# Kernel optimization log

Measured on AMD Instinct MI355X. Metric: run time of the kernel, lower is better.

Reference implementation:

```python
import jax, jax.numpy as jnp
import numpy as np

# static sinkhorn parameters (match SamplesLoss init kwargs)
P = 2
BLUR = 0.05
SCALING = 0.5
DIAMETER = 2.0  # points on the unit sphere => diameter <= 2

# geomloss epsilon_schedule: [diameter^p] + exp(arange(p*log(d), p*log(blur), p*log(scaling))) + [blur^p]
EPS_LIST = (
    [DIAMETER ** P]
    + [float(np.exp(e)) for e in np.arange(P * np.log(DIAMETER), P * np.log(BLUR), P * np.log(SCALING))]
    + [BLUR ** P]
)


def cost(m, n):
    # spherical (geodesic) distance / 2 between unit vectors: acos(<m,n>)/2
    t = jnp.clip(jnp.einsum('bnd,bmd->bnm', m, n), -1.0 + 1e-6, 1.0 - 1e-6)
    return jnp.arccos(t) * 0.5  # (B,N,M)


def softmin(eps, C, wlog):
    # -eps * logsumexp(wlog[B,1,M] - C/eps, axis=2) -> (B,N)
    return -eps * jax.nn.logsumexp(wlog[:, None, :] - C / eps, axis=2)


def log_weights(a):
    return jnp.where(a > 0, jnp.log(jnp.maximum(a, 1e-30)), -1e5)


def setup_inputs() -> dict:
    key = jax.random.key(0)
    kx, ky = jax.random.split(key)
    B, N, M, D = 8, 2048, 2048, 3
    x = jax.random.normal(kx, (B, N, D), dtype=jnp.float32)
    y = jax.random.normal(ky, (B, M, D), dtype=jnp.float32)
    # project onto the unit sphere (spherical cost assumes unit vectors)
    x = x / jnp.linalg.norm(x, axis=-1, keepdims=True)
    y = y / jnp.linalg.norm(y, axis=-1, keepdims=True)
    alpha = jnp.ones((B, N), dtype=jnp.float32) / N
    beta = jnp.ones((B, M), dtype=jnp.float32) / M
    return {"alpha": alpha, "x": x, "beta": beta, "y": y}


def reference(alpha, x, beta, y):
    sg = jax.lax.stop_gradient
    # second argument of each cost is detached, as in the torch code
    C_xx = cost(x, sg(x))
    C_yy = cost(y, sg(y))
    C_xy = cost(x, sg(y))
    C_yx = cost(y, sg(x))
    al = log_weights(alpha)
    bl = log_weights(beta)

    # ---- sinkhorn loop (torch.no_grad section) ----
    Cxx_, Cyy_, Cxy_, Cyx_, al_, bl_ = map(sg, (C_xx, C_yy, C_xy, C_yx, al, bl))
    eps = EPS_LIST[0]
    a_x = softmin(eps, Cxx_, al_)   # OT(a,a) potential on x
    b_y = softmin(eps, Cyy_, bl_)   # OT(b,b) potential on y
    a_y = softmin(eps, Cyx_, al_)   # OT(a,b) potential on y
    b_x = softmin(eps, Cxy_, bl_)   # OT(a,b) potential on x
    for eps in EPS_LIST:  # annealed, symmetrized sinkhorn updates
        at_x = softmin(eps, Cxx_, al_ + a_x / eps)
        bt_y = softmin(eps, Cyy_, bl_ + b_y / eps)
        at_y = softmin(eps, Cyx_, al_ + b_x / eps)
        bt_x = softmin(eps, Cxy_, bl_ + a_y / eps)
        a_x, b_y = 0.5 * (a_x + at_x), 0.5 * (b_y + bt_y)
        a_y, b_x = 0.5 * (a_y + at_y), 0.5 * (b_x + bt_x)

    # ---- last extrapolation, differentiable (eps = blur^p) ----
    eps = EPS_LIST[-1]
    a_x = softmin(eps, C_xx, sg(al + a_x / eps))
    b_y = softmin(eps, C_yy, sg(bl + b_y / eps))
    a_y = softmin(eps, C_yx, sg(al + b_x / eps))
    b_x = softmin(eps, C_xy, sg(bl + a_y / eps))

    # balanced (reach=None), debiased sinkhorn cost -> (B,)
    return jnp.sum(alpha * (b_x - a_x), axis=-1) + jnp.sum(beta * (a_y - b_y), axis=-1)
```

## Files before the change

### kernel.cpp

```cpp
#include <hip/hip_runtime.h>
#include <math.h>

#define BB 8
#define NN 2048
#define L2E 1.4426950408889634f
#define LN2 0.6931471805599453f
#define PI_F 3.14159265358979f
#define CLIP 0.999999f
#define THSC 20860.0f
#define THSCI (1.0f / 20860.0f)

constexpr int TB   = 128;
constexpr int T16  = NN / TB;
constexpr int NXX  = T16 * (T16 + 1) / 2;
constexpr int NT   = 2 * NXX + T16 * T16;
constexpr int SARR = BB * NN;

__device__ __forceinline__ void decode_tile(int bx, int& kind, int& I, int& J) {
    if (bx < NXX) kind = 0;
    else if (bx < 2 * NXX) { kind = 1; bx -= NXX; }
    else { kind = 2; bx -= 2 * NXX; }
    if (kind < 2) {
        int idx = bx; I = 0;
        for (;;) { int len = T16 - I; if (idx < len) { J = I + idx; break; } idx -= len; I++; }
    } else { I = bx >> 4; J = bx & 15; }
}

__device__ __forceinline__ float acos_raw(float d) {
    const float u = fabsf(d);
    float pl = fmaf(u, -0.0187293f, 0.0742610f);
    pl = fmaf(u, pl, -0.2121144f); pl = fmaf(u, pl, 1.5707288f);
    const float rt = __builtin_amdgcn_sqrtf(1.f - u) * pl;
    return (d >= 0.f) ? rt : (PI_F - rt);
}

__device__ __forceinline__ size_t th_off(int g, int wv, int lane) {
    return (size_t)(((g * 4 + wv) * 64 + lane) * 8);
}

__global__ __launch_bounds__(256)
void pack_kernel(const float* __restrict__ alpha, const float* __restrict__ beta,
                 float* __restrict__ gxw, float* __restrict__ gyw,
                 float* __restrict__ Wall, float* __restrict__ Gall,
                 float* __restrict__ out)
{
    const int tid = threadIdx.x;
    const int gid = blockIdx.x * 256 + tid;
    if (blockIdx.x == 0 && tid < BB) out[tid] = 0.f;
    const int o = gid >> 14, i = gid & (SARR - 1);
    const float* w = (o == 0 || o == 3) ? alpha : beta;
    const float v = w[i];
    const float g = ((v > 0.f) ? logf(fmaxf(v, 1e-30f)) : -1e5f) * L2E;
    if (o == 0) gxw[i] = g;
    if (o == 1) gyw[i] = g;
    float m = g;
    m = fmaxf(m, __shfl_xor(m, 1));  m = fmaxf(m, __shfl_xor(m, 2));
    m = fmaxf(m, __shfl_xor(m, 4));  m = fmaxf(m, __shfl_xor(m, 8));
    m = fmaxf(m, __shfl_xor(m, 16)); m = fmaxf(m, __shfl_xor(m, 32));
    __shared__ float wmax[4];
    const int wv = tid >> 6;
    if ((tid & 63) == 0) wmax[wv] = m;
    __syncthreads();
    const int grp = tid >> 7;
    const float G = fmaxf(wmax[grp * 2], wmax[grp * 2 + 1]);
    Wall[gid] = __builtin_amdgcn_exp2f(g - G);
    if ((tid & 127) == 0) Gall[gid >> 7] = G;
}

__global__ __launch_bounds__(256)
void maxes_kernel(const float* __restrict__ x, const float* __restrict__ y,
                  float* __restrict__ Rxx, float* __restrict__ Ryy,
                  float* __restrict__ Rxy, float* __restrict__ Cxy,
                  unsigned short* __restrict__ Theta,
                  const float* __restrict__ Wall, const float* __restrict__ Gall,
                  float2* pAX, float2* pBY, float2* pAY, float2* pBX,
                  float negK, int writeTheta)
{
    __shared__ float4 p1s[TB], p2s[TB];
    __shared__ float colred[4][TB];
    __shared__ float colpart[4][TB];
    int kind, I, J; decode_tile(blockIdx.x, kind, I, J);
    const int b = blockIdx.y, t = threadIdx.x;
    const float* P1 = (kind == 1) ? y : x;
    const float* P2 = (kind == 0) ? x : y;
    const int o1 = (kind == 0) ? 0 : (kind == 1) ? 1 : 3;
    const int o2 = (kind == 0) ? 0 : (kind == 1) ? 1 : 2;
    float2* rowOut = (kind == 0) ? pAX : (kind == 1) ? pBY : pBX;
    float2* colOut = (kind == 0) ? pAX : (kind == 1) ? pBY : pAY;
    const bool diag = (kind < 2) && (I == J);
    const float* W1 = Wall + (size_t)o1 * SARR;
    const float* W2 = Wall + (size_t)o2 * SARR;

    if (t < TB) {
        size_t gi = (size_t)b * NN + (size_t)I * TB + t;
        p1s[t] = make_float4(P1[gi * 3], P1[gi * 3 + 1], P1[gi * 3 + 2], W1[gi]);
    } else {
        int u = t - TB; size_t gi = (size_t)b * NN + (size_t)J * TB + u;
        p2s[u] = make_float4(P2[gi * 3], P2[gi * 3 + 1], P2[gi * 3 + 2], W2[gi]);
    }
    const float G1 = Gall[o1 * 128 + b * T16 + I];
    const float G2 = Gall[o2 * 128 + b * T16 + J];
    __syncthreads();
    const int lane = t & 63, wv = t >> 6, colg = lane & 7, rowg = lane >> 3;
    const int r0 = wv * 32 + rowg * 4;
    unsigned short* Tb = Theta + ((size_t)(b * NT + blockIdx.x) << 14);

    float4 pr[4];
#pragma unroll
    for (int rr = 0; rr < 4; rr++) pr[rr] = p1s[r0 + rr];
    float rmx[4] = {-2.f, -2.f, -2.f, -2.f};
    float cmx[16];
#pragma unroll
    for (int j = 0; j < 16; j++) cmx[j] = -2.f;
    float racc[4] = {0.f, 0.f, 0.f, 0.f};
    float cacc[16];
#pragma unroll
    for (int j = 0; j < 16; j++) cacc[j] = 0.f;

#pragma unroll
    for (int g = 0; g < 8; g++) {
        uint4 outv;
#pragma unroll
        for (int e = 0; e < 2; e++) {
            const int j = g * 2 + e;
            const float4 q = p2s[colg + 8 * j];
            unsigned int lo = 0, hi = 0;
#pragma unroll
            for (int rr = 0; rr < 4; rr++) {
                const float d = fmaf(pr[rr].x, q.x, fmaf(pr[rr].y, q.y, pr[rr].z * q.z));
                rmx[rr] = fmaxf(rmx[rr], d);
                cmx[j] = fmaxf(cmx[j], d);
                if (writeTheta) {
                    const float dc = fminf(fmaxf(d, -CLIP), CLIP);
                    const float th = acos_raw(dc);
                    const unsigned int qv = __float2uint_rn(th * THSC);
                    if (rr == 0) lo = qv;
                    else if (rr == 1) lo |= qv << 16;
                    else if (rr == 2) hi = qv;
                    else hi |= qv << 16;
                    const float em = __builtin_amdgcn_exp2f(th * negK);
                    racc[rr] = fmaf(q.w, em, racc[rr]);
                    cacc[j]  = fmaf(pr[rr].w, em, cacc[j]);
                }
            }
            if (e == 0) { outv.x = lo; outv.y = hi; }
            else        { outv.z = lo; outv.w = hi; }
        }
        if (writeTheta)
            *(uint4*)(Tb + th_off(g, wv, lane)) = outv;
    }

#pragma unroll
    for (int rr = 0; rr < 4; rr++) {
        float v = rmx[rr];
        v = fmaxf(v, __shfl_xor(v, 1)); v = fmaxf(v, __shfl_xor(v, 2));
        v = fmaxf(v, __shfl_xor(v, 4));
        rmx[rr] = v;
    }
    if (colg == 0) {
        float* R = (kind == 0) ? Rxx : (kind == 1) ? Ryy : Rxy;
        const size_t base = ((size_t)b * T16 + J) * NN + (size_t)I * TB + r0;
#pragma unroll
        for (int rr = 0; rr < 4; rr++)
            R[base + rr] = acos_raw(fminf(fmaxf(rmx[rr], -CLIP), CLIP));
    }
#pragma unroll
    for (int j = 0; j < 16; j++) {
        float v = cmx[j];
        v = fmaxf(v, __shfl_xor(v, 8)); v = fmaxf(v, __shfl_xor(v, 16));
        v = fmaxf(v, __shfl_xor(v, 32));
        cmx[j] = v;
    }
    if (rowg == 0) {
#pragma unroll
        for (int j = 0; j < 16; j++) colred[wv][colg + 8 * j] = cmx[j];
    }

    if (writeTheta) {
#pragma unroll
        for (int j = 0; j < 16; j++) {
            float v = cacc[j];
            v += __shfl_xor(v, 8); v += __shfl_xor(v, 16); v += __shfl_xor(v, 32);
            cacc[j] = v;
        }
        if (rowg == 0) {
#pragma unroll
            for (int j = 0; j < 16; j++) colpart[wv][colg + 8 * j] = cacc[j];
        }
#pragma unroll
        for (int rr = 0; rr < 4; rr++) {
            float v = racc[rr];
            v += __shfl_xor(v, 1); v += __shfl_xor(v, 2); v += __shfl_xor(v, 4);
            racc[rr] = v;
        }
        if (colg == 0) {
            const size_t gr = (size_t)J * SARR + (size_t)b * NN + (size_t)I * TB + r0;
#pragma unroll
            for (int rr = 0; rr < 4; rr++)
                rowOut[gr + rr] = make_float2(G2, racc[rr]);
        }
    }

    __syncthreads();
    if (t < TB) {
        const float v = fmaxf(fmaxf(colred[0][t], colred[1][t]),
                              fmaxf(colred[2][t], colred[3][t]));
        const float th = acos_raw(fminf(fmaxf(v, -CLIP), CLIP));
        if (kind == 2) {
            Cxy[((size_t)b * T16 + I) * NN + (size_t)J * TB + t] = th;
        } else if (I != J) {
            float* R = (kind == 0) ? Rxx : Ryy;
            R[((size_t)b * T16 + I) * NN + (size_t)J * TB + t] = th;
        }
        if (writeTheta && !diag) {
            const float pv = colpart[0][t] + colpart[1][t] + colpart[2][t] + colpart[3][t];
            const size_t gc = (size_t)I * SARR + (size_t)b * NN + (size_t)J * TB + t;
            colOut[gc] = make_float2(G1, pv);
        }
    }
}

struct TileArgsT {
    const unsigned short* Theta;
    const float* Wall; const float* Gall;
    const float* Rxx; const float* Ryy; const float* Rxy; const float* Cxy;
    float2* pAX; float2* pBY; float2* pAY; float2* pBX;
};

__global__ __launch_bounds__(256)
void tile_theta_kernel(TileArgsT A, float ieh, float Kq)
{
    __shared__ float2 s1[TB], s2[TB];
    __shared__ float colpart[4][TB];
    int kind, I, J; decode_tile(blockIdx.x, kind, I, J);
    const int b = blockIdx.y, t = threadIdx.x;
    const int lane = t & 63, wv = t >> 6, colg = lane & 7, rowg = lane >> 3;
    const int r0 = wv * 32 + rowg * 4;

    const unsigned short* Tb = A.Theta + ((size_t)(b * NT + blockIdx.x) << 14);
    uint4 tq[8];
#pragma unroll
    for (int g = 0; g < 8; g++) tq[g] = *(const uint4*)(Tb + th_off(g, wv, lane));

    const int o1 = (kind == 0) ? 0 : (kind == 1) ? 1 : 3;
    const int o2 = (kind == 0) ? 0 : (kind == 1) ? 1 : 2;
    float2* rowOut = (kind == 0) ? A.pAX : (kind == 1) ? A.pBY : A.pBX;
    float2* colOut = (kind == 0) ? A.pAX : (kind == 1) ? A.pBY : A.pAY;
    const bool diag = (kind < 2) && (I == J);
    const float* W1 = A.Wall + (size_t)o1 * SARR;
    const float* W2 = A.Wall + (size_t)o2 * SARR;
    const float* Rrow = (kind == 0) ? A.Rxx : (kind == 1) ? A.Ryy : A.Rxy;
    const float* Csrc = (kind == 0) ? A.Rxx : (kind == 1) ? A.Ryy : A.Cxy;

    if (t < TB) {
        size_t gi = (size_t)b * NN + (size_t)I * TB + t;
        s1[t] = make_float2(Rrow[((size_t)b * T16 + J) * NN + (size_t)I * TB + t] * ieh, W1[gi]);
    } else {
        int u = t - TB; size_t gi = (size_t)b * NN + (size_t)J * TB + u;
        s2[u] = make_float2(Csrc[((size_t)b * T16 + I) * NN + (size_t)J * TB + u] * ieh, W2[gi]);
    }
    const float G1 = A.Gall[o1 * 128 + b * T16 + I];
    const float G2 = A.Gall[o2 * 128 + b * T16 + J];
    __syncthreads();

    float srr[4], w1r[4];
#pragma unroll
    for (int rr = 0; rr < 4; rr++) { const float2 v = s1[r0 + rr]; srr[rr] = v.x; w1r[rr] = v.y; }
    float racc[4] = {0.f, 0.f, 0.f, 0.f};
    float cacc[16];
#pragma unroll
    for (int j = 0; j < 16; j++) cacc[j] = 0.f;

    if (diag) {
#pragma unroll
        for (int g = 0; g < 8; g++) {
#pragma unroll
            for (int e = 0; e < 2; e++) {
                const int j = g * 2 + e;
                const unsigned int lo = e ? tq[g].z : tq[g].x;
                const unsigned int hi = e ? tq[g].w : tq[g].y;
                const float2 sv = s2[colg + 8 * j];
                const float thv[4] = {
                    (float)(lo & 0xffffu), (float)(lo >> 16),
                    (float)(hi & 0xffffu), (float)(hi >> 16)
                };
#pragma unroll
                for (int rr = 0; rr < 4; rr++) {
                    const float er = __builtin_amdgcn_exp2f(fmaf(thv[rr], -Kq, srr[rr]));
                    racc[rr] = fmaf(sv.y, er, racc[rr]);
                }
            }
        }
    } else {
#pragma unroll
        for (int g = 0; g < 8; g++) {
#pragma unroll
            for (int e = 0; e < 2; e++) {
                const int j = g * 2 + e;
                const unsigned int lo = e ? tq[g].z : tq[g].x;
                const unsigned int hi = e ? tq[g].w : tq[g].y;
                const float2 sv = s2[colg + 8 * j];
                const float thv[4] = {
                    (float)(lo & 0xffffu), (float)(lo >> 16),
                    (float)(hi & 0xffffu), (float)(hi >> 16)
                };
#pragma unroll
                for (int rr = 0; rr < 4; rr++) {
                    const float er = __builtin_amdgcn_exp2f(fmaf(thv[rr], -Kq, srr[rr]));
                    const float ec = __builtin_amdgcn_exp2f(fmaf(thv[rr], -Kq, sv.x));
                    racc[rr] = fmaf(sv.y, er, racc[rr]);
                    cacc[j]  = fmaf(w1r[rr], ec, cacc[j]);
                }
            }
        }
    }

#pragma unroll
    for (int rr = 0; rr < 4; rr++) {
        float v = racc[rr];
        v += __shfl_xor(v, 1); v += __shfl_xor(v, 2); v += __shfl_xor(v, 4);
        racc[rr] = v;
    }
    if (colg == 0) {
        const size_t gr = (size_t)J * SARR + (size_t)b * NN + (size_t)I * TB + r0;
#pragma unroll
        for (int rr = 0; rr < 4; rr++)
            rowOut[gr + rr] = make_float2(G2 - srr[rr], racc[rr]);
    }
    if (!diag) {
#pragma unroll
        for (int j = 0; j < 16; j++) {
            float v = cacc[j];
            v += __shfl_xor(v, 8); v += __shfl_xor(v, 16); v += __shfl_xor(v, 32);
            cacc[j] = v;
        }
        if (rowg == 0) {
#pragma unroll
            for (int j = 0; j < 16; j++) colpart[wv][colg + 8 * j] = cacc[j];
        }
        __syncthreads();
        if (t < TB) {
            const float v = colpart[0][t] + colpart[1][t] + colpart[2][t] + colpart[3][t];
            const size_t gc = (size_t)I * SARR + (size_t)b * NN + (size_t)J * TB + t;
            colOut[gc] = make_float2(G1 - s2[t].x, v);
        }
    }
}

struct TileArgs {
    const float* x; const float* y;
    const float* Wall; const float* Gall;
    const float* Rxx; const float* Ryy; const float* Rxy; const float* Cxy;
    float2* pAX; float2* pBY; float2* pAY; float2* pBX;
};

__global__ __launch_bounds__(256)
void tile_kernel(TileArgs A, float ieh, float pi_ieh)
{
    __shared__ float4 p1s[TB], p2s[TB];
    __shared__ float srs[TB], scs[TB];
    __shared__ float colpart[4][TB];
    int kind, I, J; decode_tile(blockIdx.x, kind, I, J);
    const int b = blockIdx.y, t = threadIdx.x;
    const float* P1 = (kind == 1) ? A.y : A.x;
    const float* P2 = (kind == 0) ? A.x : A.y;
    const int o1 = (kind == 0) ? 0 : (kind == 1) ? 1 : 3;
    const int o2 = (kind == 0) ? 0 : (kind == 1) ? 1 : 2;
    float2* rowOut = (kind == 0) ? A.pAX : (kind == 1) ? A.pBY : A.pBX;
    float2* colOut = (kind == 0) ? A.pAX : (kind == 1) ? A.pBY : A.pAY;
    const bool diag = (kind < 2) && (I == J);
    const float* W1 = A.Wall + (size_t)o1 * SARR;
    const float* W2 = A.Wall + (size_t)o2 * SARR;
    const float* Rrow = (kind == 0) ? A.Rxx : (kind == 1) ? A.Ryy : A.Rxy;
    const float* Csrc = (kind == 0) ? A.Rxx : (kind == 1) ? A.Ryy : A.Cxy;

    const float K0 = 1.5707288f * ieh, K1 = -0.2121144f * ieh;
    const float K2 = 0.0742610f * ieh, K3 = -0.0187293f * ieh;

    if (t < TB) {
        size_t gi = (size_t)b * NN + (size_t)I * TB + t;
        p1s[t] = make_float4(P1[gi * 3], P1[gi * 3 + 1], P1[gi * 3 + 2], W1[gi]);
        srs[t] = Rrow[((size_t)b * T16 + J) * NN + (size_t)I * TB + t] * ieh;
    } else {
        int u = t - TB; size_t gi = (size_t)b * NN + (size_t)J * TB + u;
        p2s[u] = make_float4(P2[gi * 3], P2[gi * 3 + 1], P2[gi * 3 + 2], W2[gi]);
        scs[u] = Csrc[((size_t)b * T16 + I) * NN + (size_t)J * TB + u] * ieh;
    }
    const float G1 = A.Gall[o1 * 128 + b * T16 + I];
    const float G2 = A.Gall[o2 * 128 + b * T16 + J];
    __syncthreads();

    const int lane = t & 63, wv = t >> 6, colg = lane & 7, rowg = lane >> 3;
    const int r0 = wv * 32 + rowg * 4;
    float4 pr[4]; float srr[4];
#pragma unroll
    for (int rr = 0; rr < 4; rr++) { pr[rr] = p1s[r0 + rr]; srr[rr] = srs[r0 + rr]; }
    float racc[4] = {0.f, 0.f, 0.f, 0.f};
    float cacc[16];
#pragma unroll
    for (int j = 0; j < 16; j++) cacc[j] = 0.f;

#pragma unroll
    for (int j = 0; j < 16; j++) {
        const float4 q = p2s[colg + 8 * j];
        const float sc = scs[colg + 8 * j];
#pragma unroll
        for (int rr = 0; rr < 4; rr++) {
            const float4 p = pr[rr];
            float d = fmaf(p.x, q.x, fmaf(p.y, q.y, p.z * q.z));
            d = fminf(fmaxf(d, -CLIP), CLIP);
            const float u = fabsf(d);
            float pl = fmaf(u, K3, K2); pl = fmaf(u, pl, K1); pl = fmaf(u, pl, K0);
            const float rt = __builtin_amdgcn_sqrtf(1.f - u) * pl;
            const float ach = (d >= 0.f) ? rt : (pi_ieh - rt);
            racc[rr] = fmaf(q.w, __builtin_amdgcn_exp2f(srr[rr] - ach), racc[rr]);
            cacc[j]  = fmaf(p.w, __builtin_amdgcn_exp2f(sc - ach), cacc[j]);
        }
    }

#pragma unroll
    for (int j = 0; j < 16; j++) {
        float v = cacc[j];
        v += __shfl_xor(v, 8); v += __shfl_xor(v, 16); v += __shfl_xor(v, 32);
        cacc[j] = v;
    }
    if (rowg == 0) {
#pragma unroll
        for (int j = 0; j < 16; j++) colpart[wv][colg + 8 * j] = cacc[j];
    }
#pragma unroll
    for (int rr = 0; rr < 4; rr++) {
        float v = racc[rr];
        v += __shfl_xor(v, 1); v += __shfl_xor(v, 2); v += __shfl_xor(v, 4);
        racc[rr] = v;
    }
    if (colg == 0) {
        const size_t gr = (size_t)J * SARR + (size_t)b * NN + (size_t)I * TB + r0;
#pragma unroll
        for (int rr = 0; rr < 4; rr++)
            rowOut[gr + rr] = make_float2(G2 - srr[rr], racc[rr]);
    }
    __syncthreads();
    if (!diag && t < TB) {
        const float v = colpart[0][t] + colpart[1][t] + colpart[2][t] + colpart[3][t];
        const size_t gc = (size_t)I * SARR + (size_t)b * NN + (size_t)J * TB + t;
        colOut[gc] = make_float2(G1 - scs[t], v);
    }
}

__global__ __launch_bounds__(256)
void combine_kernel(const float2* __restrict__ pAX, const float2* __restrict__ pBY,
                    const float2* __restrict__ pAY, const float2* __restrict__ pBX,
                    float* __restrict__ ax, float* __restrict__ by,
                    float* __restrict__ ay, float* __restrict__ bx,
                    const float* __restrict__ gxw, const float* __restrict__ gyw,
                    float* __restrict__ Wall, float* __restrict__ Gall,
                    const float* __restrict__ alpha, const float* __restrict__ beta,
                    float* __restrict__ out,
                    float eps_ln2, float nieL2E, int do_avg, int do_out)
{
    const int tid = threadIdx.x;
    const int gid2 = blockIdx.x * 256 + tid;
    const int row = gid2 >> 1, half = gid2 & 1;
    const int o = row >> 14, i = row & (SARR - 1);
    const float2* P = (o == 0) ? pAX : (o == 1) ? pBY : (o == 2) ? pAY : pBX;
    float* pot = (o == 0) ? ax : (o == 1) ? by : (o == 2) ? ay : bx;
    float2 pr[8];
#pragma unroll
    for (int u = 0; u < 8; u++) pr[u] = P[(size_t)(half * 8 + u) * SARR + i];
    float M = -3.0e38f;
#pragma unroll
    for (int u = 0; u < 8; u++) M = fmaxf(M, (pr[u].y > 0.f) ? pr[u].x : -3.0e38f);
    float S = 0.f;
#pragma unroll
    for (int u = 0; u < 8; u++)
        S += pr[u].y * __builtin_amdgcn_exp2f(fminf(pr[u].x - M, 0.f));
    const float Mo = __shfl_xor(M, 1);
    const float So = __shfl_xor(S, 1);
    const float nm = fmaxf(M, Mo);
    S = S * __builtin_amdgcn_exp2f(M - nm) + So * __builtin_amdgcn_exp2f(Mo - nm);
    S = fmaxf(S, 1e-38f);
    float r = -eps_ln2 * (nm + __builtin_amdgcn_logf(S));
    if (do_avg) r = 0.5f * (r + pot[i]);
    if (half == 0) pot[i] = r;

    const int wv = tid >> 6;
    if (do_out) {
        float c = 0.f;
        if (half == 0) {
            const float w = ((o == 0 || o == 3) ? alpha : beta)[i];
            const float sgn = (o == 0 || o == 1) ? -1.f : 1.f;
            c = sgn * w * r;
        }
        c += __shfl_xor(c, 1);  c += __shfl_xor(c, 2);  c += __shfl_xor(c, 4);
        c += __shfl_xor(c, 8);  c += __shfl_xor(c, 16); c += __shfl_xor(c, 32);
        __shared__ float bs[4];
        if ((tid & 63) == 0) bs[wv] = c;
        __syncthreads();
        if (tid == 0) atomicAdd(&out[i >> 11], bs[0] + bs[1] + bs[2] + bs[3]);
        return;
    }

    const float g = ((o == 0 || o == 3) ? gxw[i] : gyw[i]) + r * nieL2E;
    float m = g;
    m = fmaxf(m, __shfl_xor(m, 1));  m = fmaxf(m, __shfl_xor(m, 2));
    m = fmaxf(m, __shfl_xor(m, 4));  m = fmaxf(m, __shfl_xor(m, 8));
    m = fmaxf(m, __shfl_xor(m, 16)); m = fmaxf(m, __shfl_xor(m, 32));
    __shared__ float wmax[4];
    if ((tid & 63) == 0) wmax[wv] = m;
    __syncthreads();
    const float G = fmaxf(fmaxf(wmax[0], wmax[1]), fmaxf(wmax[2], wmax[3]));
    if (half == 0) Wall[row] = __builtin_amdgcn_exp2f(g - G);
    if (tid == 0) Gall[blockIdx.x] = G;
}

extern "C" void kernel_launch(void* const* d_in, const int* in_sizes, int n_in,
                              void* d_out, int out_size, void* d_ws, size_t ws_size,
                              hipStream_t stream)
{
    const float* alpha = (const float*)d_in[0];
    const float* x     = (const float*)d_in[1];
    const float* beta  = (const float*)d_in[2];
    const float* y     = (const float*)d_in[3];
    float* out = (float*)d_out;
    float* ws  = (float*)d_ws;

    const size_t S = SARR;
    float* gxw  = ws;
    float* gyw  = ws + S;
    float* ax   = ws + 2 * S;
    float* by   = ws + 3 * S;
    float* ay   = ws + 4 * S;
    float* bx   = ws + 5 * S;
    float* Wall = ws + 6 * S;
    float* Gall = ws + 10 * S;
    float* Rxx  = ws + 10 * S + 512;
    float* Ryy  = Rxx + 16 * S;
    float* Rxy  = Ryy + 16 * S;
    float* Cxy  = Rxy + 16 * S;
    float* pb   = Cxy + 16 * S;
    const size_t PSZ = (size_t)SARR * T16;
    float2* pAX = (float2*)pb;
    float2* pBY = pAX + PSZ;
    float2* pAY = pBY + PSZ;
    float2* pBX = pAY + PSZ;

    float* thetaF = pb + (size_t)8 * PSZ;
    unsigned short* Theta = (unsigned short*)thetaF;
    const size_t used_bytes  = (size_t)((char*)thetaF - (char*)ws);
    const size_t theta_bytes = (size_t)BB * NT * 16384 * sizeof(unsigned short);
    const int useTheta = (ws_size >= used_bytes + theta_bytes) ? 1 : 0;

    const float EPS[8] = {4.0f, 4.0f, 1.0f, 0.25f, 0.0625f, 0.015625f, 0.00390625f, 0.0025f};

    pack_kernel<<<(4 * SARR) / 256, 256, 0, stream>>>(alpha, beta, gxw, gyw, Wall, Gall, out);
    const float negK = -0.5f * (1.f / EPS[0]) * L2E;
    maxes_kernel<<<dim3(NT, BB), 256, 0, stream>>>(x, y, Rxx, Ryy, Rxy, Cxy, Theta,
                                                   Wall, Gall, pAX, pBY, pAY, pBX,
                                                   negK, useTheta);

    TileArgsT TT;
    TT.Theta = Theta; TT.Wall = Wall; TT.Gall = Gall;
    TT.Rxx = Rxx; TT.Ryy = Ryy; TT.Rxy = Rxy; TT.Cxy = Cxy;
    TT.pAX = pAX; TT.pBY = pBY; TT.pAY = pAY; TT.pBX = pBX;

    TileArgs TA;
    TA.x = x; TA.y = y; TA.Wall = Wall; TA.Gall = Gall;
    TA.Rxx = Rxx; TA.Ryy = Ryy; TA.Rxy = Rxy; TA.Cxy = Cxy;
    TA.pAX = pAX; TA.pBY = pBY; TA.pAY = pAY; TA.pBX = pBX;

    auto step = [&](float e, float next_e, int avg, int run_tile, int do_out) {
        const float ieh = 0.5f * (1.f / e) * L2E;
        if (run_tile) {
            if (useTheta)
                tile_theta_kernel<<<dim3(NT, BB), 256, 0, stream>>>(TT, ieh, ieh * THSCI);
            else
                tile_kernel<<<dim3(NT, BB), 256, 0, stream>>>(TA, ieh, PI_F * ieh);
        }
        combine_kernel<<<(8 * SARR) / 256, 256, 0, stream>>>(
            pAX, pBY, pAY, pBX, ax, by, ay, bx, gxw, gyw, Wall, Gall,
            alpha, beta, out,
            e * LN2, (1.f / next_e) * L2E, avg, do_out);
    };

    step(EPS[0], EPS[0], 0, useTheta ? 0 : 1, 0);
    for (int k = 0; k < 8; k++) step(EPS[k], (k < 7) ? EPS[k + 1] : EPS[7], 1, 1, 0);
    step(EPS[7], EPS[7], 0, 1, 1);
}
```

Baseline: 415.0 us.

## Process two theta tiles per block, prefetching second tile's loads upfront

Each block of the theta tile kernel now handles two consecutive tiles. It issues the global loads for both tiles' theta data and staging values before computing the first one, so memory latency for the second tile overlaps the first tile's compute. The grid is halved and launch bounds request 3 blocks per CU. Holding both tiles' data in registers raises register pressure, and NT must be even for the pairing to cover every tile.

```diff
diff --git a/kernel.cpp b/kernel.cpp
--- a/kernel.cpp
+++ b/kernel.cpp
@@ -227,41 +227,39 @@
     float2* pAX; float2* pBY; float2* pAY; float2* pBX;
 };
 
-__global__ __launch_bounds__(256)
-void tile_theta_kernel(TileArgsT A, float ieh, float Kq)
-{
-    __shared__ float2 s1[TB], s2[TB];
-    __shared__ float colpart[4][TB];
-    int kind, I, J; decode_tile(blockIdx.x, kind, I, J);
-    const int b = blockIdx.y, t = threadIdx.x;
+__device__ __forceinline__ float2 load_stage(const TileArgsT& A, int b,
+                                             int kind, int I, int J)
+{
+    const int t = threadIdx.x;
+    const int o1 = (kind == 0) ? 0 : (kind == 1) ? 1 : 3;
+    const int o2 = (kind == 0) ? 0 : (kind == 1) ? 1 : 2;
+    const float* Rrow = (kind == 0) ? A.Rxx : (kind == 1) ? A.Ryy : A.Rxy;
+    const float* Csrc = (kind == 0) ? A.Rxx : (kind == 1) ? A.Ryy : A.Cxy;
+    if (t < TB) {
+        const size_t gi = (size_t)b * NN + (size_t)I * TB + t;
+        return make_float2(Rrow[((size_t)b * T16 + J) * NN + (size_t)I * TB + t],
+                           A.Wall[(size_t)o1 * SARR + gi]);
+    } else {
+        const int u = t - TB;
+        const size_t gi = (size_t)b * NN + (size_t)J * TB + u;
+        return make_float2(Csrc[((size_t)b * T16 + I) * NN + (size_t)J * TB + u],
+                           A.Wall[(size_t)o2 * SARR + gi]);
+    }
+}
+
+__device__ __forceinline__ void tile_compute(const TileArgsT& A, float Kq, int b,
+                                             int kind, int I, int J,
+                                             const uint4 (&tq)[8],
+                                             const float2* s1, const float2* s2,
+                                             float (&colpart)[4][TB],
+                                             float G1, float G2)
+{
+    const int t = threadIdx.x;
     const int lane = t & 63, wv = t >> 6, colg = lane & 7, rowg = lane >> 3;
     const int r0 = wv * 32 + rowg * 4;
-
-    const unsigned short* Tb = A.Theta + ((size_t)(b * NT + blockIdx.x) << 14);
-    uint4 tq[8];
-#pragma unroll
-    for (int g = 0; g < 8; g++) tq[g] = *(const uint4*)(Tb + th_off(g, wv, lane));
-
-    const int o1 = (kind == 0) ? 0 : (kind == 1) ? 1 : 3;
-    const int o2 = (kind == 0) ? 0 : (kind == 1) ? 1 : 2;
+    const bool diag = (kind < 2) && (I == J);
     float2* rowOut = (kind == 0) ? A.pAX : (kind == 1) ? A.pBY : A.pBX;
     float2* colOut = (kind == 0) ? A.pAX : (kind == 1) ? A.pBY : A.pAY;
-    const bool diag = (kind < 2) && (I == J);
-    const float* W1 = A.Wall + (size_t)o1 * SARR;
-    const float* W2 = A.Wall + (size_t)o2 * SARR;
-    const float* Rrow = (kind == 0) ? A.Rxx : (kind == 1) ? A.Ryy : A.Rxy;
-    const float* Csrc = (kind == 0) ? A.Rxx : (kind == 1) ? A.Ryy : A.Cxy;
-
-    if (t < TB) {
-        size_t gi = (size_t)b * NN + (size_t)I * TB + t;
-        s1[t] = make_float2(Rrow[((size_t)b * T16 + J) * NN + (size_t)I * TB + t] * ieh, W1[gi]);
-    } else {
-        int u = t - TB; size_t gi = (size_t)b * NN + (size_t)J * TB + u;
-        s2[u] = make_float2(Csrc[((size_t)b * T16 + I) * NN + (size_t)J * TB + u] * ieh, W2[gi]);
-    }
-    const float G1 = A.Gall[o1 * 128 + b * T16 + I];
-    const float G2 = A.Gall[o2 * 128 + b * T16 + J];
-    __syncthreads();
 
     float srr[4], w1r[4];
 #pragma unroll
@@ -345,6 +343,48 @@
             colOut[gc] = make_float2(G1 - s2[t].x, v);
         }
     }
+}
+
+__global__ __launch_bounds__(256, 3)
+void tile_theta2_kernel(TileArgsT A, float ieh, float Kq)
+{
+    __shared__ float2 s1[TB], s2[TB];
+    __shared__ float colpart[4][TB];
+    const int b = blockIdx.y, t = threadIdx.x;
+    const int t0 = 2 * blockIdx.x, t1 = t0 + 1;
+    const int lane = t & 63, wv = t >> 6;
+    int k0, I0, J0, k1, I1, J1;
+    decode_tile(t0, k0, I0, J0);
+    decode_tile(t1, k1, I1, J1);
+
+    const unsigned short* Tb0 = A.Theta + ((size_t)(b * NT + t0) << 14);
+    const unsigned short* Tb1 = A.Theta + ((size_t)(b * NT + t1) << 14);
+    uint4 tqA[8], tqB[8];
+#pragma unroll
+    for (int g = 0; g < 8; g++) tqA[g] = *(const uint4*)(Tb0 + th_off(g, wv, lane));
+    const float2 stA = load_stage(A, b, k0, I0, J0);
+#pragma unroll
+    for (int g = 0; g < 8; g++) tqB[g] = *(const uint4*)(Tb1 + th_off(g, wv, lane));
+    const float2 stB = load_stage(A, b, k1, I1, J1);
+    const int o1a = (k0 == 0) ? 0 : (k0 == 1) ? 1 : 3;
+    const int o2a = (k0 == 0) ? 0 : (k0 == 1) ? 1 : 2;
+    const int o1b = (k1 == 0) ? 0 : (k1 == 1) ? 1 : 3;
+    const int o2b = (k1 == 0) ? 0 : (k1 == 1) ? 1 : 2;
+    const float G1a = A.Gall[o1a * 128 + b * T16 + I0];
+    const float G2a = A.Gall[o2a * 128 + b * T16 + J0];
+    const float G1b = A.Gall[o1b * 128 + b * T16 + I1];
+    const float G2b = A.Gall[o2b * 128 + b * T16 + J1];
+
+    if (t < TB) s1[t] = make_float2(stA.x * ieh, stA.y);
+    else        s2[t - TB] = make_float2(stA.x * ieh, stA.y);
+    __syncthreads();
+    tile_compute(A, Kq, b, k0, I0, J0, tqA, s1, s2, colpart, G1a, G2a);
+    __syncthreads();
+
+    if (t < TB) s1[t] = make_float2(stB.x * ieh, stB.y);
+    else        s2[t - TB] = make_float2(stB.x * ieh, stB.y);
+    __syncthreads();
+    tile_compute(A, Kq, b, k1, I1, J1, tqB, s1, s2, colpart, G1b, G2b);
 }
 
 struct TileArgs {
@@ -573,7 +613,7 @@
         const float ieh = 0.5f * (1.f / e) * L2E;
         if (run_tile) {
             if (useTheta)
-                tile_theta_kernel<<<dim3(NT, BB), 256, 0, stream>>>(TT, ieh, ieh * THSCI);
+                tile_theta2_kernel<<<dim3(NT / 2, BB), 256, 0, stream>>>(TT, ieh, ieh * THSCI);
             else
                 tile_kernel<<<dim3(NT, BB), 256, 0, stream>>>(TA, ieh, PI_F * ieh);
         }
```

After: 528.4 us. +27.3%, slower.
